# Optimization experiments

Measured on AMD Instinct MI355X. Metric: run time of the kernel, lower is better.

Reference implementation:

```python
import jax, jax.numpy as jnp
import numpy as np

EPS = 1e-8
LN_EPS = 1e-5
TOPK = 8

B, N, D = 8, 2048, 512


def setup_inputs() -> dict:
    key = jax.random.key(0)
    ks = jax.random.split(key, 4)
    feats = jax.random.normal(ks[0], (B, N, D), dtype=jnp.float32)
    mask = jnp.ones((B, N), dtype=bool)
    # per-layer GCN weights (no bias) and LayerNorm params, plus output LN
    W1 = jax.random.normal(ks[1], (D, D), dtype=jnp.float32) / np.sqrt(D)
    W2 = jax.random.normal(ks[2], (D, D), dtype=jnp.float32) / np.sqrt(D)
    ln1_g = jnp.ones((D,), jnp.float32); ln1_b = jnp.zeros((D,), jnp.float32)
    ln2_g = jnp.ones((D,), jnp.float32); ln2_b = jnp.zeros((D,), jnp.float32)
    out_g = jnp.ones((D,), jnp.float32); out_b = jnp.zeros((D,), jnp.float32)
    return {"feats": feats, "mask": mask, "W1": W1, "ln1_g": ln1_g, "ln1_b": ln1_b,
            "W2": W2, "ln2_g": ln2_g, "ln2_b": ln2_b, "out_g": out_g, "out_b": out_b}


def _layer_norm(x, g, b):
    mu = jnp.mean(x, axis=-1, keepdims=True)
    var = jnp.mean(jnp.square(x - mu), axis=-1, keepdims=True)
    return (x - mu) * jax.lax.rsqrt(var + LN_EPS) * g + b


def build_similarity_graph(feats, mask):
    b, n, _ = feats.shape
    mask_f = mask.astype(feats.dtype)                       # [B,N]
    valid_pair = mask[:, None, :] & mask[:, :, None]        # [B,N,N]
    vp_f = valid_pair.astype(feats.dtype)
    # cosine similarity mapped to [0,1]
    fn = feats / jnp.clip(jnp.linalg.norm(feats, axis=-1, keepdims=True), EPS)
    sim = (jnp.einsum('bnd,bmd->bnm', fn, fn) + 1.0) * 0.5
    sim = sim * vp_f
    eye = jnp.eye(n, dtype=bool)
    sim_wo_self = jnp.where(eye[None], 0.0, sim)
    # top-k neighbors per node (invalid pairs pushed to -1)
    k = min(TOPK, n - 1)
    candidate = jnp.where(valid_pair, sim_wo_self, -1.0)
    values, indices = jax.lax.top_k(candidate, k)           # [B,N,k]
    bi = jnp.arange(b)[:, None, None]
    ri = jnp.arange(n)[None, :, None]
    knn_mask = jnp.zeros((b, n, n), dtype=bool).at[bi, ri, indices].set(values > 0)
    adj = sim_wo_self * knn_mask.astype(feats.dtype)
    # symmetrize, add valid self-loops, re-mask
    adj = 0.5 * (adj + jnp.swapaxes(adj, 1, 2))
    adj = adj + jnp.eye(n, dtype=feats.dtype)[None] * (mask_f[:, :, None] * mask_f[:, None, :])
    adj = adj * vp_f
    # symmetric degree normalization
    deg_inv_sqrt = jnp.clip(adj.sum(-1), EPS) ** -0.5       # [B,N]
    adj_norm = adj * deg_inv_sqrt[:, :, None] * deg_inv_sqrt[:, None, :]
    return adj_norm * vp_f


def _gcn_layer(x, adj_norm, W, g, b, mask_f):
    out = jnp.einsum('bnm,bmd->bnd', adj_norm, x @ W) + x   # residual (Identity proj)
    out = jax.nn.relu(_layer_norm(out, g, b))
    return out * mask_f[..., None]


def reference(feats, mask, W1, ln1_g, ln1_b, W2, ln2_g, ln2_b, out_g, out_b):
    mask_f = mask.astype(feats.dtype)
    x = feats * mask_f[..., None]                           # input_proj = Identity, then mask
    adj_norm = build_similarity_graph(feats, mask)
    x = _gcn_layer(x, adj_norm, W1, ln1_g, ln1_b, mask_f)
    x = _gcn_layer(x, adj_norm, W2, ln2_g, ln2_b, mask_f)
    x = _layer_norm(x, out_g, out_b)
    return x * mask_f[..., None]
```

## Files before the change

kernel.cpp:

```cpp
#include <hip/hip_runtime.h>
#include <cstdint>


constexpr int Bb   = 8;
constexpr int Nn   = 2048;
constexpr int Dd   = 512;
constexpr int BN   = Bb * Nn;
constexpr int KTOP = 8;
constexpr int CAP  = 56;
constexpr int NSLICE = 8;

typedef __attribute__((ext_vector_type(8))) __bf16 bf16x8;
typedef __attribute__((ext_vector_type(4))) __bf16 bf16x4;
typedef __attribute__((ext_vector_type(4))) float  f32x4;

__device__ __forceinline__ void gload16(const void* g, void* l) {
  __builtin_amdgcn_global_load_lds((const __attribute__((address_space(1))) unsigned int*)g,
                                   (__attribute__((address_space(3))) unsigned int*)l,
                                   16, 0, 0);
}
__device__ __forceinline__ void barrier_raw() {
  asm volatile("" ::: "memory");
  __builtin_amdgcn_s_barrier();
  asm volatile("" ::: "memory");
}
__device__ __forceinline__ unsigned umax_(unsigned a, unsigned b) { return a > b ? a : b; }
__device__ __forceinline__ unsigned umin_(unsigned a, unsigned b) { return a > b ? b : a; }

__global__ __launch_bounds__(256) void prep_kernel(const float* __restrict__ feats,
                                                   float* __restrict__ rinv,
                                                   float* __restrict__ normv,
                                                   __bf16* __restrict__ Hk,
                                                   int* __restrict__ ecnt,
                                                   const float* __restrict__ W1,
                                                   const float* __restrict__ W2,
                                                   __bf16* __restrict__ Wk1,
                                                   __bf16* __restrict__ Wk2) {
  __shared__ float tile[64][65];
  __shared__ float rsh[64];
  const int t = threadIdx.x;

  if (blockIdx.x >= 256) {
    const int idx = blockIdx.x - 256;
    const float* W = (idx >> 8) ? W2 : W1;
    __bf16* Wk     = (idx >> 8) ? Wk2 : Wk1;
    const int rem = idx & 255;
    const int bx = (rem & 15) * 32, by = (rem >> 4) * 32;
    float (*tt)[33] = (float(*)[33])tile;
    const int lx = t & 31, ly = t >> 5;
#pragma unroll
    for (int r = 0; r < 32; r += 8)
      tt[ly + r][lx] = W[(size_t)(by + ly + r) * Dd + bx + lx];
    __syncthreads();
    if (t < 128) {
      const int k8l = t >> 5, nl = t & 31;
      bf16x8 v;
#pragma unroll
      for (int e = 0; e < 8; ++e) v[e] = (__bf16)tt[k8l * 8 + e][nl];
      *(bf16x8*)(Wk + ((size_t)((by >> 3) + k8l) * Dd + bx + nl) * 8) = v;
    }
    return;
  }

  const int r0 = blockIdx.x * 64;
  const int bz = r0 >> 11;
  const int n0 = r0 & 2047;
  const int wv = t >> 6, lane = t & 63;

  if (t < 64) ecnt[r0 + t] = 0;

  for (int i = 0; i < 16; ++i) {
    const int row = wv * 16 + i;
    const float* p = feats + (size_t)(r0 + row) * Dd + lane * 8;
    float4 a = *(const float4*)p;
    float4 b = *(const float4*)(p + 4);
    float s = a.x*a.x + a.y*a.y + a.z*a.z + a.w*a.w
            + b.x*b.x + b.y*b.y + b.z*b.z + b.w*b.w;
#pragma unroll
    for (int o = 32; o; o >>= 1) s += __shfl_down(s, o);
    if (lane == 0) {
      const float nr = fmaxf(sqrtf(s), 1e-8f);
      rsh[row] = 1.0f / nr;
      rinv[r0 + row]  = 1.0f / nr;
      normv[r0 + row] = nr;
    }
  }

  for (int kt = 0; kt < 8; ++kt) {
    __syncthreads();
#pragma unroll
    for (int p = 0; p < 4; ++p) {
      const int row = p * 16 + (t >> 4), ch = t & 15;
      float4 v = *(const float4*)(feats + (size_t)(r0 + row) * Dd + kt * 64 + ch * 4);
      tile[row][ch * 4 + 0] = v.x; tile[row][ch * 4 + 1] = v.y;
      tile[row][ch * 4 + 2] = v.z; tile[row][ch * 4 + 3] = v.w;
    }
    __syncthreads();
#pragma unroll
    for (int h = 0; h < 2; ++h) {
      const int c = h * 256 + t;
      const int k8l = c >> 6, row = c & 63;
      const float s = rsh[row];
      bf16x8 hv;
#pragma unroll
      for (int e = 0; e < 8; ++e) hv[e] = (__bf16)(tile[row][k8l * 8 + e] * s);
      *(bf16x8*)(Hk + ((size_t)(bz * 64) + (size_t)(kt * 8 + k8l)) * (Nn * 8)
                    + (n0 + row) * 8) = hv;
    }
  }
}

__device__ __forceinline__ void ins8t(float (&tv)[8], int (&ti)[8], float v, int idx) {
#pragma unroll
  for (int q = 0; q < 8; ++q) {
    bool sw = (v > tv[q]) || (v == tv[q] && idx < ti[q]);
    float a = sw ? tv[q] : v;
    int   c = sw ? ti[q] : idx;
    tv[q] = sw ? v   : tv[q];
    ti[q] = sw ? idx : ti[q];
    v = a; idx = c;
  }
}

__global__ __launch_bounds__(256, 4) void sim_hh_topk(const __bf16* __restrict__ Hk,
                                                      float* __restrict__ pv,
                                                      int* __restrict__ pi) {
  __shared__ __align__(16) char smem[32768];

  const int f     = blockIdx.x;
  const int bz    = f & 7;
  const int rr    = f >> 3;
  const int r0    = (rr & 15) * 128;
  const int slice = rr >> 4;

  const int tid    = threadIdx.x;
  const int lane   = tid & 63;
  const int lane15 = tid & 15;
  const int kgrp   = (tid >> 4) & 3;
  const int wv     = tid >> 6;
  const int wrow0  = wv * 32;
  const int bN     = bz * Nn;

  const __bf16* Hb = Hk + (size_t)(bz * 64) * (Nn * 8);

  unsigned t8k[2][8];
#pragma unroll
  for (int rs = 0; rs < 2; ++rs)
#pragma unroll
    for (int q = 0; q < 8; ++q) t8k[rs][q] = 0u;

  auto stage = [&](int t, int buf) {
    const int ct = t >> 4, k80 = (t & 15) << 2;
    const int c0 = slice * 256 + ct * 128;
#pragma unroll
    for (int i = 0; i < 4; ++i) {
      const int c = (wv << 2) + i;
      const bool isB = c >= 8;
      const int cc = isB ? c - 8 : c;
      const int kg = cc >> 1, rb = cc & 1;
      const int rbase = (isB ? c0 : r0) + rb * 64 + lane;
      gload16(Hb + ((size_t)(k80 + kg) * Nn + rbase) * 8,
              smem + buf * 16384 + (isB ? 8192 : 0) + kg * 2048 + (rb * 64 + lane) * 16);
    }
  };

  f32x4 acc[2][8];
  const f32x4 z = {0.f, 0.f, 0.f, 0.f};

  stage(0, 0);
  for (int t = 0; t < 32; ++t) {
    const int cur = t & 1;
    if ((t & 15) == 0) {
#pragma unroll
      for (int i = 0; i < 2; ++i)
#pragma unroll
        for (int j = 0; j < 8; ++j) acc[i][j] = z;
    }
    if (t + 1 < 32) {
      stage(t + 1, cur ^ 1);
      asm volatile("s_waitcnt vmcnt(4)" ::: "memory");
    } else {
      asm volatile("s_waitcnt vmcnt(0)" ::: "memory");
    }
    barrier_raw();

    const char* sb = smem + cur * 16384;
    const int a0o = kgrp * 2048 + (wrow0 + lane15) * 16;
    bf16x8 ah0 = *(const bf16x8*)(sb + a0o);
    bf16x8 ah1 = *(const bf16x8*)(sb + a0o + 256);
#pragma unroll
    for (int cs = 0; cs < 8; ++cs) {
      bf16x8 bh = *(const bf16x8*)(sb + 8192 + kgrp * 2048 + (cs * 16 + lane15) * 16);
      acc[0][cs] = __builtin_amdgcn_mfma_f32_16x16x32_bf16(bh, ah0, acc[0][cs], 0, 0, 0);
      acc[1][cs] = __builtin_amdgcn_mfma_f32_16x16x32_bf16(bh, ah1, acc[1][cs], 0, 0, 0);
    }
    barrier_raw();

    if ((t & 15) == 15) {
      const int ctile0 = slice * 256 + (t >> 4) * 128;
#pragma unroll
      for (int rs = 0; rs < 2; ++rs) {
        const int rowg = r0 + wrow0 + rs * 16 + lane15;
#pragma unroll
        for (int cs = 0; cs < 8; ++cs) {
          const int colb = ctile0 + cs * 16 + kgrp * 4;
#pragma unroll
          for (int e = 0; e < 4; ++e) {
            const int col = colb + e;
            unsigned key = (__float_as_uint(acc[rs][cs][e] + 2.0f) & 0xFFFFF800u)
                         | (unsigned)(0x7FF - col);
            key = (col == rowg) ? 0u : key;
#pragma unroll
            for (int q = 0; q < 8; ++q) {
              const unsigned hi = umax_(t8k[rs][q], key);
              key = umin_(t8k[rs][q], key);
              t8k[rs][q] = hi;
            }
          }
        }
      }
    }
  }

#pragma unroll
  for (int rs = 0; rs < 2; ++rs) {
#pragma unroll
    for (int m = 16; m <= 32; m <<= 1) {
      unsigned ok[8];
#pragma unroll
      for (int q = 0; q < 8; ++q) ok[q] = (unsigned)__shfl_xor((int)t8k[rs][q], m);
#pragma unroll
      for (int q = 0; q < 8; ++q) {
        unsigned key = ok[q];
#pragma unroll
        for (int p = 0; p < 8; ++p) {
          const unsigned hi = umax_(t8k[rs][p], key);
          key = umin_(t8k[rs][p], key);
          t8k[rs][p] = hi;
        }
      }
    }
  }

  if (lane < 16) {
#pragma unroll
    for (int rs = 0; rs < 2; ++rs) {
      const int prow = bN + r0 + wrow0 + rs * 16 + lane15;
#pragma unroll
      for (int q = 0; q < 8; ++q) {
        const unsigned key = t8k[rs][q];
        const int col = 0x7FF - (int)(key & 0x7FFu);
        const float raw = __uint_as_float(key & 0xFFFFF800u) - 2.0f;
        pv[((size_t)prow * NSLICE + slice) * 8 + q] = fmaxf((raw + 1.0f) * 0.5f, 0.0f);
        pi[((size_t)prow * NSLICE + slice) * 8 + q] = bN + col;
      }
    }
  }
}

__global__ __launch_bounds__(256) void refine_edges(const float* __restrict__ feats,
                                                    const float* __restrict__ rinv,
                                                    const float* __restrict__ pv,
                                                    const int* __restrict__ pi,
                                                    int* __restrict__ ecnt,
                                                    int* __restrict__ eidx,
                                                    float* __restrict__ ew) {
  const int f  = blockIdx.x;
  const int bz = f & 7;
  const int wv = threadIdx.x >> 6;
  const int lane = threadIdx.x & 63;
  const int bN = bz * Nn;
  const int row = bN + (f >> 3) * 4 + wv;

  const float scr = pv[(size_t)row * 64 + lane];
  const int   sid = pi[(size_t)row * 64 + lane];
  unsigned key = (__float_as_uint(scr) & 0xFFFFF800u) | (unsigned)(0x7FF - (sid - bN));

  const float* xi = feats + (size_t)row * Dd + lane * 8;
  const float4 xi0 = *(const float4*)xi;
  const float4 xi1 = *(const float4*)(xi + 4);
  const float  ri  = rinv[row];

  int ridx[12];
#pragma unroll
  for (int c = 0; c < 12; ++c) {
    unsigned m = key;
#pragma unroll
    for (int o = 32; o; o >>= 1) {
      const unsigned om = __shfl_xor(m, o);
      m = om > m ? om : m;
    }
    if (key == m) key = 0u;
    ridx[c] = bN + (0x7FF - (int)(m & 0x7FFu));
  }

  float rv[12];
#pragma unroll
  for (int c = 0; c < 12; c += 2) {
    const float* xa = feats + (size_t)ridx[c]     * Dd + lane * 8;
    const float* xb = feats + (size_t)ridx[c + 1] * Dd + lane * 8;
    const float4 a0 = *(const float4*)xa;
    const float4 a1 = *(const float4*)(xa + 4);
    const float4 b0 = *(const float4*)xb;
    const float4 b1 = *(const float4*)(xb + 4);
    float da = xi0.x*a0.x + xi0.y*a0.y + xi0.z*a0.z + xi0.w*a0.w
             + xi1.x*a1.x + xi1.y*a1.y + xi1.z*a1.z + xi1.w*a1.w;
    float db = xi0.x*b0.x + xi0.y*b0.y + xi0.z*b0.z + xi0.w*b0.w
             + xi1.x*b1.x + xi1.y*b1.y + xi1.z*b1.z + xi1.w*b1.w;
#pragma unroll
    for (int o = 32; o; o >>= 1) { da += __shfl_xor(da, o); db += __shfl_xor(db, o); }
    rv[c]     = (da * ri * rinv[ridx[c]]     + 1.0f) * 0.5f;
    rv[c + 1] = (db * ri * rinv[ridx[c + 1]] + 1.0f) * 0.5f;
  }

  float t8v[8]; int t8i[8];
#pragma unroll
  for (int q = 0; q < 8; ++q) { t8v[q] = -1.0f; t8i[q] = 0x7fffffff; }
#pragma unroll
  for (int c = 0; c < 12; ++c) ins8t(t8v, t8i, rv[c], ridx[c]);

  if (lane == 0) {
#pragma unroll
    for (int q = 0; q < KTOP; ++q) {
      if (t8v[q] > 0.0f) {
        const int j = t8i[q];
        const float w = 0.5f * t8v[q];
        int p = atomicAdd(&ecnt[row], 1);
        if (p < CAP) { eidx[row * CAP + p] = j; ew[row * CAP + p] = w; }
        int q2 = atomicAdd(&ecnt[j], 1);
        if (q2 < CAP) { eidx[j * CAP + q2] = row; ew[j * CAP + q2] = w; }
      }
    }
  }
}

__global__ __launch_bounds__(256) void deg_kernel(const int* __restrict__ ecnt,
                                                  const float* __restrict__ ew,
                                                  const float* __restrict__ normv,
                                                  float* __restrict__ dis,
                                                  float* __restrict__ dn) {
  const int r = blockIdx.x * 256 + threadIdx.x;
  if (r >= BN) return;
  const int cnt = min(ecnt[r], CAP);
  float d = 1.0f;
  for (int e = 0; e < cnt; ++e) d += ew[r * CAP + e];
  const float di = rsqrtf(fmaxf(d, 1e-8f));
  dis[r] = di;
  dn[r]  = di * normv[r];
}

template <bool BATCHED_A>
__global__ __launch_bounds__(128, 2) void gemm_mfma(const __bf16* __restrict__ Ak,
                                                    const __bf16* __restrict__ Wk,
                                                    __bf16* __restrict__ Yb) {
  __shared__ __align__(16) char smem[24576];
  const int tid    = threadIdx.x;
  const int lane   = tid & 63;
  const int lane15 = tid & 15;
  const int kgrp   = (tid >> 4) & 3;
  const int wv     = tid >> 6;
  const int m0 = blockIdx.x * 64, n0 = blockIdx.y * 128;
  const __bf16* Ab = BATCHED_A
      ? Ak + (size_t)((m0 >> 11) * 64) * (Nn * 8)
      : Ak;
  const int mloc = BATCHED_A ? (m0 & 2047) : m0;
  const int Astr = BATCHED_A ? Nn : BN;

  auto stage = [&](int t, int buf) {
    const int k80 = t << 2;
#pragma unroll
    for (int i = 0; i < 6; ++i) {
      const int c = wv * 6 + i;
      const bool isB = c >= 4;
      const int kg = isB ? (c - 4) >> 1 : c;
      const int rb = isB ? (c - 4) & 1 : 0;
      const __bf16* g = isB
          ? Wk + ((size_t)(k80 + kg) * Dd + n0 + rb * 64 + lane) * 8
          : Ab + ((size_t)(k80 + kg) * Astr + mloc + lane) * 8;
      char* d = smem + buf * 12288 +
                (isB ? 4096 + kg * 2048 + (rb * 64 + lane) * 16
                     : kg * 1024 + lane * 16);
      gload16(g, d);
    }
  };

  f32x4 acc[2][8];
  const f32x4 z = {0.f, 0.f, 0.f, 0.f};
#pragma unroll
  for (int i = 0; i < 2; ++i)
#pragma unroll
    for (int j = 0; j < 8; ++j) acc[i][j] = z;

  stage(0, 0);
  for (int t = 0; t < 16; ++t) {
    const int cur = t & 1;
    if (t + 1 < 16) {
      stage(t + 1, cur ^ 1);
      asm volatile("s_waitcnt vmcnt(6)" ::: "memory");
    } else {
      asm volatile("s_waitcnt vmcnt(0)" ::: "memory");
    }
    barrier_raw();

    const char* sb = smem + cur * 12288;
    const int a0o = kgrp * 1024 + (wv * 32 + lane15) * 16;
    bf16x8 a0 = *(const bf16x8*)(sb + a0o);
    bf16x8 a1 = *(const bf16x8*)(sb + a0o + 256);
#pragma unroll
    for (int cs = 0; cs < 8; ++cs) {
      bf16x8 b = *(const bf16x8*)(sb + 4096 + kgrp * 2048 + (cs * 16 + lane15) * 16);
      acc[0][cs] = __builtin_amdgcn_mfma_f32_16x16x32_bf16(b, a0, acc[0][cs], 0, 0, 0);
      acc[1][cs] = __builtin_amdgcn_mfma_f32_16x16x32_bf16(b, a1, acc[1][cs], 0, 0, 0);
    }
    barrier_raw();
  }
#pragma unroll
  for (int rs = 0; rs < 2; ++rs) {
    const int row = m0 + wv * 32 + rs * 16 + lane15;
#pragma unroll
    for (int cs = 0; cs < 8; ++cs) {
      bf16x4 o;
#pragma unroll
      for (int e = 0; e < 4; ++e) o[e] = (__bf16)acc[rs][cs][e];
      *(bf16x4*)(Yb + (size_t)row * Dd + n0 + cs * 16 + kgrp * 4) = o;
    }
  }
}

__device__ __forceinline__ void breduce2_128(float& s, float& q, float* red) {
#pragma unroll
  for (int o = 32; o; o >>= 1) { s += __shfl_down(s, o); q += __shfl_down(q, o); }
  __syncthreads();
  if ((threadIdx.x & 63) == 0) {
    red[(threadIdx.x >> 6) * 2]     = s;
    red[(threadIdx.x >> 6) * 2 + 1] = q;
  }
  __syncthreads();
  s = red[0] + red[2];
  q = red[1] + red[3];
}

template <bool FINAL>
__global__ __launch_bounds__(128) void agg_ln_kernel(const __bf16* __restrict__ yb,
                                                     const float* __restrict__ xres_f,
                                                     const __bf16* __restrict__ xres_k,
                                                     const int* __restrict__ ecnt,
                                                     const int* __restrict__ eidx,
                                                     const float* __restrict__ ew,
                                                     const float* __restrict__ dis,
                                                     const float* __restrict__ dwv,
                                                     const float* __restrict__ g1,
                                                     const float* __restrict__ b1v,
                                                     const float* __restrict__ g2,
                                                     const float* __restrict__ b2v,
                                                     float* __restrict__ outf,
                                                     __bf16* __restrict__ outk) {
  __shared__ float red[4];
  const int row = (blockIdx.x & 7) * Nn + (blockIdx.x >> 3);
  const int tid = threadIdx.x;
  const int d0 = tid * 4;
  const float di = dis[row];
  const float swt = di * dwv[row];

  bf16x4 yv = *(const bf16x4*)(yb + (size_t)row * Dd + d0);
  float a[4];
#pragma unroll
  for (int e2 = 0; e2 < 4; ++e2) a[e2] = swt * (float)yv[e2];

  const int cnt = min(ecnt[row], CAP);
  int e = 0;
  for (; e + 2 <= cnt; e += 2) {
    const int j0 = eidx[row * CAP + e];
    const int j1 = eidx[row * CAP + e + 1];
    const float c0 = ew[row * CAP + e]     * di * dwv[j0];
    const float c1 = ew[row * CAP + e + 1] * di * dwv[j1];
    bf16x4 v0 = *(const bf16x4*)(yb + (size_t)j0 * Dd + d0);
    bf16x4 v1 = *(const bf16x4*)(yb + (size_t)j1 * Dd + d0);
#pragma unroll
    for (int e2 = 0; e2 < 4; ++e2) a[e2] += c0 * (float)v0[e2] + c1 * (float)v1[e2];
  }
  if (e < cnt) {
    const int j = eidx[row * CAP + e];
    const float c = ew[row * CAP + e] * di * dwv[j];
    bf16x4 v = *(const bf16x4*)(yb + (size_t)j * Dd + d0);
#pragma unroll
    for (int e2 = 0; e2 < 4; ++e2) a[e2] += c * (float)v[e2];
  }

  if (FINAL) {
    bf16x4 u = *(const bf16x4*)(xres_k + ((size_t)(tid >> 1) * BN + row) * 8 + (tid & 1) * 4);
#pragma unroll
    for (int e2 = 0; e2 < 4; ++e2) a[e2] += (float)u[e2];
  } else {
    float4 xv = *(const float4*)(xres_f + (size_t)row * Dd + d0);
    a[0] += xv.x; a[1] += xv.y; a[2] += xv.z; a[3] += xv.w;
  }

  float s = a[0] + a[1] + a[2] + a[3];
  float qq = a[0]*a[0] + a[1]*a[1] + a[2]*a[2] + a[3]*a[3];
  breduce2_128(s, qq, red);
  const float mu = s * (1.0f / Dd);
  const float var = qq * (1.0f / Dd) - mu * mu;
  const float rs = rsqrtf(var + 1e-5f);
  float4 g = *(const float4*)(g1 + d0);
  float4 bb = *(const float4*)(b1v + d0);
  float tv[4];
  tv[0] = fmaxf((a[0] - mu) * rs * g.x + bb.x, 0.0f);
  tv[1] = fmaxf((a[1] - mu) * rs * g.y + bb.y, 0.0f);
  tv[2] = fmaxf((a[2] - mu) * rs * g.z + bb.z, 0.0f);
  tv[3] = fmaxf((a[3] - mu) * rs * g.w + bb.w, 0.0f);

  if (FINAL) {
    float s2 = tv[0] + tv[1] + tv[2] + tv[3];
    float q2 = tv[0]*tv[0] + tv[1]*tv[1] + tv[2]*tv[2] + tv[3]*tv[3];
    breduce2_128(s2, q2, red);
    const float mu2 = s2 * (1.0f / Dd);
    const float var2 = q2 * (1.0f / Dd) - mu2 * mu2;
    const float rs2 = rsqrtf(var2 + 1e-5f);
    float4 g2v = *(const float4*)(g2 + d0);
    float4 b2 = *(const float4*)(b2v + d0);
    float4 o;
    o.x = (tv[0] - mu2) * rs2 * g2v.x + b2.x;
    o.y = (tv[1] - mu2) * rs2 * g2v.y + b2.y;
    o.z = (tv[2] - mu2) * rs2 * g2v.z + b2.z;
    o.w = (tv[3] - mu2) * rs2 * g2v.w + b2.w;
    *(float4*)(outf + (size_t)row * Dd + d0) = o;
  } else {
    bf16x4 ov;
#pragma unroll
    for (int e2 = 0; e2 < 4; ++e2) ov[e2] = (__bf16)tv[e2];
    *(bf16x4*)(outk + ((size_t)(tid >> 1) * BN + row) * 8 + (tid & 1) * 4) = ov;
  }
}

extern "C" void kernel_launch(void* const* d_in, const int* in_sizes, int n_in,
                              void* d_out, int out_size, void* d_ws, size_t ws_size,
                              hipStream_t stream) {
  const float* feats = (const float*)d_in[0];
  const float* W1    = (const float*)d_in[2];
  const float* ln1_g = (const float*)d_in[3];
  const float* ln1_b = (const float*)d_in[4];
  const float* W2    = (const float*)d_in[5];
  const float* ln2_g = (const float*)d_in[6];
  const float* ln2_b = (const float*)d_in[7];
  const float* out_g = (const float*)d_in[8];
  const float* out_b = (const float*)d_in[9];
  float* out = (float*)d_out;

  char* w = (char*)d_ws;
  float* rinv  = (float*)w; w += (size_t)BN * 4;
  float* normv = (float*)w; w += (size_t)BN * 4;
  int*   ecnt  = (int*)w;   w += (size_t)BN * 4;
  int*   eidx  = (int*)w;   w += (size_t)BN * CAP * 4;
  float* ew    = (float*)w; w += (size_t)BN * CAP * 4;
  float* dis   = (float*)w; w += (size_t)BN * 4;
  float* dn    = (float*)w; w += (size_t)BN * 4;
  __bf16* Wk1  = (__bf16*)w; w += (size_t)Dd * Dd * 2;
  __bf16* Wk2  = (__bf16*)w; w += (size_t)Dd * Dd * 2;
  __bf16* Hk   = (__bf16*)w; w += (size_t)BN * Dd * 2;
  __bf16* Yb   = (__bf16*)w; w += (size_t)BN * Dd * 2;
  __bf16* h1k  = (__bf16*)w; w += (size_t)BN * Dd * 2;
  float* pv  = (float*)h1k;
  int*   pi  = (int*)((char*)h1k + (size_t)BN * NSLICE * 8 * 4);

  prep_kernel<<<768, 256, 0, stream>>>(feats, rinv, normv, Hk, ecnt,
                                       W1, W2, Wk1, Wk2);

  sim_hh_topk<<<1024, 256, 0, stream>>>(Hk, pv, pi);
  refine_edges<<<BN / 4, 256, 0, stream>>>(feats, rinv, pv, pi, ecnt, eidx, ew);
  deg_kernel<<<BN / 256, 256, 0, stream>>>(ecnt, ew, normv, dis, dn);

  gemm_mfma<true><<<dim3(BN / 64, Dd / 128), 128, 0, stream>>>(Hk, Wk1, Yb);
  agg_ln_kernel<false><<<BN, 128, 0, stream>>>(Yb, feats, nullptr, ecnt, eidx, ew,
                                               dis, dn, ln1_g, ln1_b,
                                               nullptr, nullptr, nullptr, h1k);
  gemm_mfma<false><<<dim3(BN / 64, Dd / 128), 128, 0, stream>>>(h1k, Wk2, Yb);
  agg_ln_kernel<true><<<BN, 128, 0, stream>>>(Yb, nullptr, h1k, ecnt, eidx, ew,
                                              dis, dis, ln2_g, ln2_b,
                                              out_g, out_b, out, nullptr);
}
```

Measured before the change: 291.4 us.

## Fuse first-layer GEMM into similarity top-k launch and enlarge GEMM tiles

The layer-1 feature GEMM (H·W1) now runs as extra blocks inside the similarity/top-k kernel. The two independent workloads share one launch, which removes a launch and lets the GEMM fill idle CUs. Both GEMMs move to 128x128 tiles with 256 threads in place of 64x128 with 128 threads, which improves operand reuse but cuts the number of blocks. The aggregation loop is unrolled to four neighbours per iteration to keep more gathers in flight. The risks are load imbalance inside the mixed kernel and the GEMM blocks competing with top-k blocks for occupancy.

```diff
diff --git a/kernel.cpp b/kernel.cpp
--- a/kernel.cpp
+++ b/kernel.cpp
@@ -122,18 +122,95 @@
   }
 }
 
-__global__ __launch_bounds__(256, 4) void sim_hh_topk(const __bf16* __restrict__ Hk,
-                                                      float* __restrict__ pv,
-                                                      int* __restrict__ pi) {
+__device__ __forceinline__ void gemm_core(const __bf16* __restrict__ Ab, int Astr, int mloc,
+                                          const __bf16* __restrict__ Wk, int m0, int n0,
+                                          __bf16* __restrict__ Yb, int tid, char* smem) {
+  const int lane   = tid & 63;
+  const int lane15 = tid & 15;
+  const int kgrp   = (tid >> 4) & 3;
+  const int wv     = tid >> 6;
+  const int wrow0  = wv * 32;
+
+  auto stage = [&](int t, int buf) {
+    const int k80 = t << 2;
+#pragma unroll
+    for (int i = 0; i < 4; ++i) {
+      const int c = (wv << 2) + i;
+      const bool isB = c >= 8;
+      const int cc = isB ? c - 8 : c;
+      const int kg = cc >> 1, rb = cc & 1;
+      const __bf16* g = isB
+          ? Wk + ((size_t)(k80 + kg) * Dd + n0 + rb * 64 + lane) * 8
+          : Ab + ((size_t)(k80 + kg) * Astr + mloc + rb * 64 + lane) * 8;
+      gload16(g, smem + buf * 16384 + (isB ? 8192 : 0) + kg * 2048 + (rb * 64 + lane) * 16);
+    }
+  };
+
+  f32x4 acc[2][8];
+  const f32x4 z = {0.f, 0.f, 0.f, 0.f};
+#pragma unroll
+  for (int i = 0; i < 2; ++i)
+#pragma unroll
+    for (int j = 0; j < 8; ++j) acc[i][j] = z;
+
+  stage(0, 0);
+  for (int t = 0; t < 16; ++t) {
+    const int cur = t & 1;
+    if (t + 1 < 16) {
+      stage(t + 1, cur ^ 1);
+      asm volatile("s_waitcnt vmcnt(4)" ::: "memory");
+    } else {
+      asm volatile("s_waitcnt vmcnt(0)" ::: "memory");
+    }
+    barrier_raw();
+
+    const char* sb = smem + cur * 16384;
+    const int a0o = kgrp * 2048 + (wrow0 + lane15) * 16;
+    bf16x8 a0 = *(const bf16x8*)(sb + a0o);
+    bf16x8 a1 = *(const bf16x8*)(sb + a0o + 256);
+#pragma unroll
+    for (int cs = 0; cs < 8; ++cs) {
+      bf16x8 b = *(const bf16x8*)(sb + 8192 + kgrp * 2048 + (cs * 16 + lane15) * 16);
+      acc[0][cs] = __builtin_amdgcn_mfma_f32_16x16x32_bf16(b, a0, acc[0][cs], 0, 0, 0);
+      acc[1][cs] = __builtin_amdgcn_mfma_f32_16x16x32_bf16(b, a1, acc[1][cs], 0, 0, 0);
+    }
+    barrier_raw();
+  }
+#pragma unroll
+  for (int rs = 0; rs < 2; ++rs) {
+    const int row = m0 + wv * 32 + rs * 16 + lane15;
+#pragma unroll
+    for (int cs = 0; cs < 8; ++cs) {
+      bf16x4 o;
+#pragma unroll
+      for (int e = 0; e < 4; ++e) o[e] = (__bf16)acc[rs][cs][e];
+      *(bf16x4*)(Yb + (size_t)row * Dd + n0 + cs * 16 + kgrp * 4) = o;
+    }
+  }
+}
+
+__global__ __launch_bounds__(256, 4) void sim_gemm_kernel(const __bf16* __restrict__ Hk,
+                                                          const __bf16* __restrict__ Wk1,
+                                                          __bf16* __restrict__ Yb,
+                                                          float* __restrict__ pv,
+                                                          int* __restrict__ pi) {
   __shared__ __align__(16) char smem[32768];
-
-  const int f     = blockIdx.x;
+  const int tid = threadIdx.x;
+
+  if (blockIdx.x < 512) {
+    const int gb = blockIdx.x;
+    const int m0 = (gb >> 2) * 128, n0 = (gb & 3) * 128;
+    const __bf16* Ab = Hk + (size_t)((m0 >> 11) * 64) * (Nn * 8);
+    gemm_core(Ab, Nn, m0 & 2047, Wk1, m0, n0, Yb, tid, smem);
+    return;
+  }
+
+  const int f     = blockIdx.x - 512;
   const int bz    = f & 7;
   const int rr    = f >> 3;
   const int r0    = (rr & 15) * 128;
   const int slice = rr >> 4;
 
-  const int tid    = threadIdx.x;
   const int lane   = tid & 63;
   const int lane15 = tid & 15;
   const int kgrp   = (tid >> 4) & 3;
@@ -256,6 +333,15 @@
       }
     }
   }
+}
+
+__global__ __launch_bounds__(256, 4) void gemm2_kernel(const __bf16* __restrict__ Ak,
+                                                       const __bf16* __restrict__ Wk,
+                                                       __bf16* __restrict__ Yb) {
+  __shared__ __align__(16) char smem[32768];
+  const int gb = blockIdx.x;
+  const int m0 = (gb >> 2) * 128, n0 = (gb & 3) * 128;
+  gemm_core(Ak, BN, m0, Wk, m0, n0, Yb, threadIdx.x, smem);
 }
 
 __global__ __launch_bounds__(256) void refine_edges(const float* __restrict__ feats,
@@ -347,84 +433,6 @@
   const float di = rsqrtf(fmaxf(d, 1e-8f));
   dis[r] = di;
   dn[r]  = di * normv[r];
-}
-
-template <bool BATCHED_A>
-__global__ __launch_bounds__(128, 2) void gemm_mfma(const __bf16* __restrict__ Ak,
-                                                    const __bf16* __restrict__ Wk,
-                                                    __bf16* __restrict__ Yb) {
-  __shared__ __align__(16) char smem[24576];
-  const int tid    = threadIdx.x;
-  const int lane   = tid & 63;
-  const int lane15 = tid & 15;
-  const int kgrp   = (tid >> 4) & 3;
-  const int wv     = tid >> 6;
-  const int m0 = blockIdx.x * 64, n0 = blockIdx.y * 128;
-  const __bf16* Ab = BATCHED_A
-      ? Ak + (size_t)((m0 >> 11) * 64) * (Nn * 8)
-      : Ak;
-  const int mloc = BATCHED_A ? (m0 & 2047) : m0;
-  const int Astr = BATCHED_A ? Nn : BN;
-
-  auto stage = [&](int t, int buf) {
-    const int k80 = t << 2;
-#pragma unroll
-    for (int i = 0; i < 6; ++i) {
-      const int c = wv * 6 + i;
-      const bool isB = c >= 4;
-      const int kg = isB ? (c - 4) >> 1 : c;
-      const int rb = isB ? (c - 4) & 1 : 0;
-      const __bf16* g = isB
-          ? Wk + ((size_t)(k80 + kg) * Dd + n0 + rb * 64 + lane) * 8
-          : Ab + ((size_t)(k80 + kg) * Astr + mloc + lane) * 8;
-      char* d = smem + buf * 12288 +
-                (isB ? 4096 + kg * 2048 + (rb * 64 + lane) * 16
-                     : kg * 1024 + lane * 16);
-      gload16(g, d);
-    }
-  };
-
-  f32x4 acc[2][8];
-  const f32x4 z = {0.f, 0.f, 0.f, 0.f};
-#pragma unroll
-  for (int i = 0; i < 2; ++i)
-#pragma unroll
-    for (int j = 0; j < 8; ++j) acc[i][j] = z;
-
-  stage(0, 0);
-  for (int t = 0; t < 16; ++t) {
-    const int cur = t & 1;
-    if (t + 1 < 16) {
-      stage(t + 1, cur ^ 1);
-      asm volatile("s_waitcnt vmcnt(6)" ::: "memory");
-    } else {
-      asm volatile("s_waitcnt vmcnt(0)" ::: "memory");
-    }
-    barrier_raw();
-
-    const char* sb = smem + cur * 12288;
-    const int a0o = kgrp * 1024 + (wv * 32 + lane15) * 16;
-    bf16x8 a0 = *(const bf16x8*)(sb + a0o);
-    bf16x8 a1 = *(const bf16x8*)(sb + a0o + 256);
-#pragma unroll
-    for (int cs = 0; cs < 8; ++cs) {
-      bf16x8 b = *(const bf16x8*)(sb + 4096 + kgrp * 2048 + (cs * 16 + lane15) * 16);
-      acc[0][cs] = __builtin_amdgcn_mfma_f32_16x16x32_bf16(b, a0, acc[0][cs], 0, 0, 0);
-      acc[1][cs] = __builtin_amdgcn_mfma_f32_16x16x32_bf16(b, a1, acc[1][cs], 0, 0, 0);
-    }
-    barrier_raw();
-  }
-#pragma unroll
-  for (int rs = 0; rs < 2; ++rs) {
-    const int row = m0 + wv * 32 + rs * 16 + lane15;
-#pragma unroll
-    for (int cs = 0; cs < 8; ++cs) {
-      bf16x4 o;
-#pragma unroll
-      for (int e = 0; e < 4; ++e) o[e] = (__bf16)acc[rs][cs][e];
-      *(bf16x4*)(Yb + (size_t)row * Dd + n0 + cs * 16 + kgrp * 4) = o;
-    }
-  }
 }
 
 __device__ __forceinline__ void breduce2_128(float& s, float& q, float* red) {
@@ -469,17 +477,25 @@
 
   const int cnt = min(ecnt[row], CAP);
   int e = 0;
-  for (; e + 2 <= cnt; e += 2) {
+  for (; e + 4 <= cnt; e += 4) {
     const int j0 = eidx[row * CAP + e];
     const int j1 = eidx[row * CAP + e + 1];
+    const int j2 = eidx[row * CAP + e + 2];
+    const int j3 = eidx[row * CAP + e + 3];
     const float c0 = ew[row * CAP + e]     * di * dwv[j0];
     const float c1 = ew[row * CAP + e + 1] * di * dwv[j1];
+    const float c2 = ew[row * CAP + e + 2] * di * dwv[j2];
+    const float c3 = ew[row * CAP + e + 3] * di * dwv[j3];
     bf16x4 v0 = *(const bf16x4*)(yb + (size_t)j0 * Dd + d0);
     bf16x4 v1 = *(const bf16x4*)(yb + (size_t)j1 * Dd + d0);
-#pragma unroll
-    for (int e2 = 0; e2 < 4; ++e2) a[e2] += c0 * (float)v0[e2] + c1 * (float)v1[e2];
-  }
-  if (e < cnt) {
+    bf16x4 v2 = *(const bf16x4*)(yb + (size_t)j2 * Dd + d0);
+    bf16x4 v3 = *(const bf16x4*)(yb + (size_t)j3 * Dd + d0);
+#pragma unroll
+    for (int e2 = 0; e2 < 4; ++e2)
+      a[e2] += c0 * (float)v0[e2] + c1 * (float)v1[e2]
+             + c2 * (float)v2[e2] + c3 * (float)v3[e2];
+  }
+  for (; e < cnt; ++e) {
     const int j = eidx[row * CAP + e];
     const float c = ew[row * CAP + e] * di * dwv[j];
     bf16x4 v = *(const bf16x4*)(yb + (size_t)j * Dd + d0);
@@ -566,15 +582,15 @@
   prep_kernel<<<768, 256, 0, stream>>>(feats, rinv, normv, Hk, ecnt,
                                        W1, W2, Wk1, Wk2);
 
-  sim_hh_topk<<<1024, 256, 0, stream>>>(Hk, pv, pi);
+  sim_gemm_kernel<<<1536, 256, 0, stream>>>(Hk, Wk1, Yb, pv, pi);
+
   refine_edges<<<BN / 4, 256, 0, stream>>>(feats, rinv, pv, pi, ecnt, eidx, ew);
   deg_kernel<<<BN / 256, 256, 0, stream>>>(ecnt, ew, normv, dis, dn);
 
-  gemm_mfma<true><<<dim3(BN / 64, Dd / 128), 128, 0, stream>>>(Hk, Wk1, Yb);
   agg_ln_kernel<false><<<BN, 128, 0, stream>>>(Yb, feats, nullptr, ecnt, eidx, ew,
                                                dis, dn, ln1_g, ln1_b,
                                                nullptr, nullptr, nullptr, h1k);
-  gemm_mfma<false><<<dim3(BN / 64, Dd / 128), 128, 0, stream>>>(h1k, Wk2, Yb);
+  gemm2_kernel<<<512, 256, 0, stream>>>(h1k, Wk2, Yb);
   agg_ln_kernel<true><<<BN, 128, 0, stream>>>(Yb, nullptr, h1k, ecnt, eidx, ew,
                                               dis, dis, ln2_g, ln2_b,
                                               out_g, out_b, out, nullptr);
```

After: 280.1 us. 1.04x faster.
